# Performance work log

Hardware: AMD Instinct MI355X
Metric: run time of the kernel (lower is better)

Reference implementation:

```python
import jax, jax.numpy as jnp
import numpy as np

N_SEQ, T, IN, H, A = 256, 512, 128, 256, 32


def setup_inputs() -> dict:
    key = jax.random.key(0)
    ks = jax.random.split(key, 10)
    s = lambda k, sh: (jax.random.normal(k, sh, dtype=jnp.float32) * 0.05)
    features = jax.random.normal(ks[0], (N_SEQ * T, IN), dtype=jnp.float32)
    episode_starts = (jax.random.uniform(ks[1], (N_SEQ * T,)) < 0.02).astype(jnp.float32)
    h0 = jnp.zeros((1, N_SEQ, H), jnp.float32)
    c0 = jnp.zeros((1, N_SEQ, H), jnp.float32)
    return dict(
        features=features, episode_starts=episode_starts, h0=h0, c0=c0,
        W_ih=s(ks[2], (4 * H, IN)), W_hh=s(ks[3], (4 * H, H)),
        b_ih=s(ks[4], (4 * H,)), b_hh=s(ks[5], (4 * H,)),
        W_logit=s(ks[6], (A, H)), b_logit=s(ks[7], (A,)),
        W_value=s(ks[8], (1, H)), b_value=s(ks[9], (1,)),
    )


def _lstm_scan(x_seq, starts, h0, c0, W_ih, W_hh, b_ih, b_hh):
    # x_seq: (T, n_seq, IN); starts: (T, n_seq); h0/c0: (n_seq, H)
    # Precompute input projection once (big GEMM), recurrence only does h @ W_hh.
    x_proj = jnp.einsum('tbi,gi->tbg', x_seq, W_ih) + b_ih + b_hh  # (T, n_seq, 4H)

    def step(carry, inp):
        h, c = carry
        xp, st = inp
        m = (1.0 - st)[:, None]          # reset states at episode starts
        h = h * m
        c = c * m
        gates = xp + h @ W_hh.T          # (n_seq, 4H)
        i, f, g, o = jnp.split(gates, 4, axis=-1)  # PyTorch gate order i,f,g,o
        c = jax.nn.sigmoid(f) * c + jax.nn.sigmoid(i) * jnp.tanh(g)
        h = jax.nn.sigmoid(o) * jnp.tanh(c)
        return (h, c), h

    (h, c), ys = jax.lax.scan(step, (h0, c0), (x_proj, starts))
    return ys, h, c


def reference(features, episode_starts, h0, c0, W_ih, W_hh, b_ih, b_hh,
              W_logit, b_logit, W_value, b_value):
    n_seq = h0.shape[1]
    in_size = W_ih.shape[1]
    x_seq = features.reshape(n_seq, -1, in_size).swapaxes(0, 1)   # (T, n_seq, IN)
    starts = episode_starts.reshape(n_seq, -1).swapaxes(0, 1)     # (T, n_seq)
    ys, h, c = _lstm_scan(x_seq, starts, h0[0], c0[0], W_ih, W_hh, b_ih, b_hh)
    out = ys.swapaxes(0, 1).reshape(-1, ys.shape[-1])             # (n_seq*T, H)
    logits = out @ W_logit.T + b_logit                            # (n_seq*T, A)
    value = out @ W_value.T + b_value                             # (n_seq*T, 1)
    return logits, value, h[None], c[None]
```

## Files before the change

kernel.cpp:

```cpp
#include <hip/hip_runtime.h>
#include <hip/hip_bf16.h>


typedef float f32x4 __attribute__((ext_vector_type(4)));
typedef int   i32x4 __attribute__((ext_vector_type(4)));
typedef short s16x8 __attribute__((ext_vector_type(8)));
typedef short s16x4 __attribute__((ext_vector_type(4)));
typedef unsigned short u16x4 __attribute__((ext_vector_type(4)));

#define L2E   1.44269504088896340736f
#define L2E2  2.88539008177792681472f

__device__ __forceinline__ float fexp2(float x) {
#if __has_builtin(__builtin_amdgcn_exp2f)
  return __builtin_amdgcn_exp2f(x);
#else
  float r; asm("v_exp_f32 %0, %1" : "=v"(r) : "v"(x)); return r;
#endif
}
__device__ __forceinline__ float frcp(float x) { return __builtin_amdgcn_rcpf(x); }
__device__ __forceinline__ float bf2f(unsigned short u) {
  return __uint_as_float(((unsigned)u) << 16);
}
__device__ __forceinline__ unsigned short f2bf(float f) {
  unsigned int b = __float_as_uint(f);
  return (unsigned short)((b + 0x7FFFu + ((b >> 16) & 1u)) >> 16);
}

__global__ void k0_quant(const float* __restrict__ Whh,
                         const float* __restrict__ Wlog,
                         const float* __restrict__ Wval,
                         signed char* __restrict__ Wq, float* __restrict__ wsc,
                         signed char* __restrict__ Wlq, float* __restrict__ lsc) {
  int r = blockIdx.x, l = threadIdx.x;
  const float* src; signed char* dst; float* sd;
  if (r < 1024) { src = Whh + (size_t)r * 256; dst = Wq + (size_t)r * 256; sd = wsc + r; }
  else {
    int hr = r - 1024;
    src = (hr < 32) ? (Wlog + (size_t)hr * 256) : Wval;
    dst = Wlq + (size_t)hr * 256; sd = lsc + hr;
  }
  f32x4 v = *(const f32x4*)(src + l * 4);
  float m = fmaxf(fmaxf(fabsf(v.x), fabsf(v.y)), fmaxf(fabsf(v.z), fabsf(v.w)));
  #pragma unroll
  for (int off = 32; off; off >>= 1) m = fmaxf(m, __shfl_xor(m, off));
  float inv = (m > 0.f) ? (127.f / m) : 0.f;
  int q0 = (int)rintf(v.x * inv), q1 = (int)rintf(v.y * inv);
  int q2 = (int)rintf(v.z * inv), q3 = (int)rintf(v.w * inv);
  unsigned int pk = (q0 & 255) | ((q1 & 255) << 8) | ((q2 & 255) << 16) | ((q3 & 255) << 24);
  *(unsigned int*)(dst + l * 4) = pk;
  if (l == 0) *sd = m * (1.f / 127.f);
}

__device__ __forceinline__ void k1_body(int gk, char* smem,
                                        const float* __restrict__ feat,
                                        const float* __restrict__ Wih,
                                        const float* __restrict__ bih,
                                        const float* __restrict__ bhh,
                                        unsigned short* __restrict__ xp, int t0) {
  short (*Bl)[136] = (short (*)[136])smem;
  float* bias = (float*)(smem + 34816);
  const int tid = threadIdx.x;
  const int bm = gk >> 3, bn = gk & 7;
  const int m0 = bm << 7, j0 = bn << 5;
  const int tg = t0 + (bm >> 1), sbase = (bm & 1) << 7;
  #pragma unroll
  for (int it = 0; it < 8; ++it) {
    int idx = it * 512 + tid;
    int rr = idx >> 5, c4 = (idx & 31) << 2;
    int g = ((rr & 3) << 8) + j0 + (rr >> 2);
    f32x4 v = *(const f32x4*)(Wih + (size_t)g * 128 + c4);
    s16x4 pk = { (short)f2bf(v.x), (short)f2bf(v.y), (short)f2bf(v.z), (short)f2bf(v.w) };
    *(s16x4*)&Bl[rr][c4] = pk;
  }
  if (tid < 128) {
    int g = ((tid & 3) << 8) + j0 + (tid >> 2);
    bias[tid] = bih[g] + bhh[g];
  }
  const int w = tid >> 6, l = tid & 63;
  const int lr = l & 15, lk8 = (l >> 4) << 3;
  s16x8 a[4];
  {
    const float* fp = feat + ((size_t)(sbase + (w << 4) + lr) * 512 + tg) * 128 + lk8;
    #pragma unroll
    for (int kk = 0; kk < 4; ++kk) {
      f32x4 v0 = *(const f32x4*)(fp + kk * 32);
      f32x4 v1 = *(const f32x4*)(fp + kk * 32 + 4);
      s16x8 pk = { (short)f2bf(v0.x), (short)f2bf(v0.y), (short)f2bf(v0.z), (short)f2bf(v0.w),
                   (short)f2bf(v1.x), (short)f2bf(v1.y), (short)f2bf(v1.z), (short)f2bf(v1.w) };
      a[kk] = pk;
    }
  }
  __syncthreads();
  f32x4 z = {0.f, 0.f, 0.f, 0.f};
  f32x4 acc[8];
  #pragma unroll
  for (int nt = 0; nt < 8; ++nt) acc[nt] = z;
  #pragma unroll
  for (int kk = 0; kk < 4; ++kk) {
    #pragma unroll
    for (int nt = 0; nt < 8; ++nt) {
      s16x8 bb = *(const s16x8*)&Bl[nt * 16 + lr][kk * 32 + lk8];
      acc[nt] = __builtin_amdgcn_mfma_f32_16x16x32_bf16(a[kk], bb, acc[nt], 0, 0, 0);
    }
  }
  #pragma unroll
  for (int nt = 0; nt < 8; ++nt) {
    #pragma unroll
    for (int r = 0; r < 4; ++r) {
      int m = m0 + (w << 4) + (l >> 4) * 4 + r;
      int c = nt * 16 + lr;
      float gsc = ((c & 3) == 2) ? L2E2 : -L2E;
      float val = (acc[nt][r] + bias[c]) * gsc;
      xp[(size_t)m * 1024 + (j0 << 2) + c] = f2bf(val);
    }
  }
}

__device__ __forceinline__ void k2_body(int bid, char* smem,
                                        const unsigned short* __restrict__ xp,
                                        const signed char* __restrict__ Wq,
                                        const float* __restrict__ wsc,
                                        const float* __restrict__ ep,
                                        const float* __restrict__ h0,
                                        const float* __restrict__ c0,
                                        float* __restrict__ hstate,
                                        float* __restrict__ cstate,
                                        signed char* __restrict__ hbuf,
                                        float* __restrict__ out, int t0, int tc) {
  __builtin_amdgcn_s_setprio(3);
  signed char (*Hl)[4][272] = (signed char (*)[4][272])smem;
  float* flgl = (float*)(smem + 2176);
  const int tid = threadIdx.x;
  const int w = tid >> 6, l = tid & 63;
  const int lc = l & 15, lq = l >> 4;
  const int hf = lq >> 1;
  const int odd = lq & 1;
  const int sb2 = odd << 1;
  const int j = (w << 5) + (hf << 4) + lc;
  const int s0 = bid << 2;
  const bool last = (t0 + tc == 512);

  {
    const float* hsrc = (t0 == 0) ? h0 : hstate;
    #pragma unroll
    for (int it = 0; it < 2; ++it) {
      int idx = it * 512 + tid;
      int s = idx >> 8, jj = idx & 255;
      float v = hsrc[(size_t)(s0 + s) * 256 + jj];
      float q = rintf(fminf(fmaxf(v * 127.f, -127.f), 127.f));
      Hl[0][s][jj] = (signed char)(int)q;
    }
  }
  {
    int n = tc << 2;
    for (int idx = tid; idx < n; idx += 512) {
      int s = idx & 3, llt = idx >> 2;
      flgl[idx] = ep[(size_t)(s0 + s) * 512 + t0 + llt];
    }
  }

  i32x4 wq[8][4];
  #pragma unroll
  for (int tau = 0; tau < 8; ++tau) {
    int g = (tau >> 1) * 256 + (w << 5) + ((tau & 1) << 4) + lc;
    #pragma unroll
    for (int kk = 0; kk < 4; ++kk)
      wq[tau][kk] = *(const i32x4*)(Wq + (size_t)g * 256 + kk * 64 + (lq << 4));
  }
  float dsc[4];
  #pragma unroll
  for (int gamma = 0; gamma < 4; ++gamma) {
    float sgn = (gamma == 2) ? L2E2 : -L2E;
    dsc[gamma] = sgn * wsc[gamma * 256 + j] * (1.f / 127.f);
  }

  float cst[2];
  {
    const float* csrc = (t0 == 0) ? c0 : cstate;
    #pragma unroll
    for (int cc = 0; cc < 2; ++cc)
      cst[cc] = csrc[(size_t)(s0 + sb2 + cc) * 256 + j];
  }

  const size_t xoff = ((size_t)(s0 + sb2) * 256 + j) * 4;
  u16x4 xqA[2], xqB[2];
  {
    const unsigned short* pp = xp + xoff;
    #pragma unroll
    for (int cc = 0; cc < 2; ++cc) xqA[cc] = *(const u16x4*)(pp + cc * 1024);
  }
  __syncthreads();

  const int aoff = (lc & 3) * 272 + (lq << 4);
  const i32x4 zero4 = {0, 0, 0, 0};

#define STEP(HR, HWR, XC, XN, LT)                                              \
  {                                                                            \
    const int lt_ = (LT);                                                      \
    if (lt_ + 1 < tc) {                     \
      const unsigned short* pp = xp + (size_t)(lt_ + 1) * 262144 + xoff;       \
      _Pragma("unroll")                                                        \
      for (int cc = 0; cc < 2; ++cc) XN[cc] = *(const u16x4*)(pp + cc * 1024); \
    }                                                                          \
    float fa = flgl[lt_ * 4 + (lc & 3)];          \
    i32x4 racc[8];                                                             \
    const signed char* hbase = &(HR)[0][0];                                    \
    {                                                                          \
      i32x4 a = *(const i32x4*)(hbase + aoff);                                 \
      i32x4 am = (fa != 0.f) ? zero4 : a;                                      \
      _Pragma("unroll")                                                        \
      for (int tau = 0; tau < 8; ++tau)                                        \
        racc[tau] = __builtin_amdgcn_mfma_i32_16x16x64_i8(am, wq[tau][0], zero4, 0, 0, 0); \
    }                                                                          \
    _Pragma("unroll")                                                          \
    for (int kk = 1; kk < 4; ++kk) {                                           \
      i32x4 a = *(const i32x4*)(hbase + aoff + kk * 64);                       \
      i32x4 am = (fa != 0.f) ? zero4 : a;                                      \
      _Pragma("unroll")                                                        \
      for (int tau = 0; tau < 8; ++tau)                                        \
        racc[tau] = __builtin_amdgcn_mfma_i32_16x16x64_i8(am, wq[tau][kk], racc[tau], 0, 0, 0); \
    }                                                                          \
    i32x4 sg0 = hf ? racc[1] : racc[0];         \
    i32x4 sg1 = hf ? racc[3] : racc[2];                                        \
    i32x4 sg2 = hf ? racc[5] : racc[4];                                        \
    i32x4 sg3 = hf ? racc[7] : racc[6];                                        \
    signed char* hw = &(HWR)[0][0];                                            \
    signed char* hb = hbuf + ((size_t)lt_ * 256 + (s0 + sb2)) * 256 + j;       \
    _Pragma("unroll")                                                          \
    for (int cc = 0; cc < 2; ++cc) {                                           \
      int g0 = odd ? sg0[2 + cc] : sg0[cc];                                    \
      int g1 = odd ? sg1[2 + cc] : sg1[cc];                                    \
      int g2 = odd ? sg2[2 + cc] : sg2[cc];                                    \
      int g3 = odd ? sg3[2 + cc] : sg3[cc];                                    \
      u16x4 xv = XC[cc];                                                       \
      float xi = fmaf((float)g0, dsc[0], bf2f(xv.x));                          \
      float xf = fmaf((float)g1, dsc[1], bf2f(xv.y));                          \
      float xg = fmaf((float)g2, dsc[2], bf2f(xv.z));                          \
      float xo = fmaf((float)g3, dsc[3], bf2f(xv.w));                          \
      float si = frcp(1.f + fexp2(xi));                                        \
      float sf = frcp(1.f + fexp2(xf));                                        \
      float so = frcp(1.f + fexp2(xo));                                        \
      float tg = fmaf(-2.f, frcp(1.f + fexp2(xg)), 1.f);                       \
      float fr = flgl[lt_ * 4 + sb2 + cc];                                     \
      float cp = (fr != 0.f) ? 0.f : cst[cc];                                  \
      float cn = fmaf(sf, cp, si * tg);                                        \
      cst[cc] = cn;                                                            \
      float th = fmaf(-2.f, frcp(1.f + fexp2(L2E2 * cn)), 1.f);                \
      float hn = so * th;                                                      \
      signed char q8 = (signed char)(int)rintf(hn * 127.f);                    \
      hw[(sb2 + cc) * 272 + j] = q8;                                           \
      hb[cc * 256] = q8;                                                       \
      if (lt_ == tc - 1) {                                                     \
        int sg = s0 + sb2 + cc;                                                \
        hstate[(size_t)sg * 256 + j] = hn;                                     \
        cstate[(size_t)sg * 256 + j] = cn;                                     \
        if (last) {                                                            \
          out[4325376 + (size_t)sg * 256 + j] = hn;                            \
          out[4390912 + (size_t)sg * 256 + j] = cn;                            \
        }                                                                      \
      }                                                                        \
    }                                                                          \
    asm volatile("s_waitcnt lgkmcnt(0)\n\ts_barrier" ::: "memory");            \
  }

  for (int lt = 0; lt < tc; lt += 2) {
    STEP(Hl[0], Hl[1], xqA, xqB, lt);
    STEP(Hl[1], Hl[0], xqB, xqA, lt + 1);
  }
#undef STEP
}

__device__ __forceinline__ void k3_body(int gk,
                                        const signed char* __restrict__ hbuf,
                                        const signed char* __restrict__ Wlq,
                                        const float* __restrict__ lsc,
                                        const float* __restrict__ blog,
                                        const float* __restrict__ bval,
                                        float* __restrict__ out,
                                        int t0, int tc, int tcsh) {
  const int w = threadIdx.x >> 6, l = threadIdx.x & 63;
  const int lc = l & 15, lq = l >> 4;
  const int tk = gk * 8 + w;
  const int pg = tk >> tcsh, lt = tk & (tc - 1);
  const int t = t0 + lt;
  const i32x4 zero4 = {0, 0, 0, 0};

  i32x4 dacc[3] = {zero4, zero4, zero4};
  #pragma unroll
  for (int kk = 0; kk < 4; ++kk) {
    i32x4 a = *(const i32x4*)(hbuf + ((size_t)lt * 256 + (pg << 4) + lc) * 256
                              + kk * 64 + (lq << 4));
    #pragma unroll
    for (int n = 0; n < 3; ++n) {
      int row = n * 16 + lc;
      i32x4 bf = (row < 33) ? *(const i32x4*)(Wlq + (size_t)row * 256 + kk * 64 + (lq << 4))
                            : zero4;
      dacc[n] = __builtin_amdgcn_mfma_i32_16x16x64_i8(a, bf, dacc[n], 0, 0, 0);
    }
  }
  #pragma unroll
  for (int n = 0; n < 2; ++n) {
    float dsn = lsc[n * 16 + lc] * (1.f / 127.f);
    float lbn = blog[n * 16 + lc];
    #pragma unroll
    for (int r = 0; r < 4; ++r) {
      int sg = (pg << 4) + lq * 4 + r;
      out[((size_t)sg * 512 + t) * 32 + n * 16 + lc] = fmaf((float)dacc[n][r], dsn, lbn);
    }
  }
  if (lc == 0) {
    float ds2 = lsc[32] * (1.f / 127.f);
    float b2 = bval[0];
    #pragma unroll
    for (int r = 0; r < 4; ++r) {
      int sg = (pg << 4) + lq * 4 + r;
      out[4194304 + (size_t)sg * 512 + t] = fmaf((float)dacc[2][r], ds2, b2);
    }
  }
}

__launch_bounds__(512, 2)
__global__ void mega(int nk2, int t0_2, const unsigned short* xp2, signed char* hb2,
                     int nk1, int t0_1, unsigned short* xp1,
                     int nk3, int t0_3, const signed char* hb3,
                     const float* feat, const float* Wih,
                     const float* bih, const float* bhh,
                     const signed char* Wq, const float* wsc,
                     const signed char* Wlq, const float* lsc,
                     const float* ep, const float* h0, const float* c0,
                     const float* blog, const float* bval,
                     float* hstate, float* cstate, float* out,
                     int tc, int tcsh) {
  __shared__ __align__(16) char smem[81920];
  int bid = (int)blockIdx.x;
  if (bid < nk2) {
    k2_body(bid, smem, xp2, Wq, wsc, ep, h0, c0, hstate, cstate, hb2, out, t0_2, tc);
  } else if (bid < nk2 + nk1) {
    k1_body(bid - nk2, smem, feat, Wih, bih, bhh, xp1, t0_1);
  } else {
    k3_body(bid - nk2 - nk1, hb3, Wlq, lsc, blog, bval, out, t0_3, tc, tcsh);
  }
}

extern "C" void kernel_launch(void* const* d_in, const int* in_sizes, int n_in,
                              void* d_out, int out_size, void* d_ws, size_t ws_size,
                              hipStream_t stream) {
  const float* feat = (const float*)d_in[0];
  const float* ep   = (const float*)d_in[1];
  const float* h0   = (const float*)d_in[2];
  const float* c0   = (const float*)d_in[3];
  const float* Wih  = (const float*)d_in[4];
  const float* Whh  = (const float*)d_in[5];
  const float* bih  = (const float*)d_in[6];
  const float* bhh  = (const float*)d_in[7];
  const float* Wlog = (const float*)d_in[8];
  const float* blog = (const float*)d_in[9];
  const float* Wval = (const float*)d_in[10];
  const float* bval = (const float*)d_in[11];
  float* out = (float*)d_out;
  char* ws = (char*)d_ws;
  signed char* Wq     = (signed char*)(ws + 0);
  float*       wsc    = (float*)      (ws + 262144);
  signed char* Wlq    = (signed char*)(ws + 266240);
  float*       lsc    = (float*)      (ws + 274688);
  float*       hstate = (float*)      (ws + 275456);
  float*       cstate = (float*)      (ws + 537600);

  int Tc = 128;
  while (Tc > 16 && (size_t)1048576 + (size_t)Tc * 1179648 > ws_size) Tc >>= 1;
  int tcsh = 31 - __builtin_clz(Tc);
  int nc = 512 / Tc;
  size_t xpsz = (size_t)Tc * 524288, hbsz = (size_t)Tc * 65536;
  unsigned short* xpb[2] = { (unsigned short*)(ws + 1048576),
                             (unsigned short*)(ws + 1048576 + xpsz) };
  signed char*    hbb[2] = { (signed char*)(ws + 1048576 + 2 * xpsz),
                             (signed char*)(ws + 1048576 + 2 * xpsz + hbsz) };
  const int NK1 = Tc * 16;
  const int NK3 = Tc * 2;
  const int NK2 = 64;

  hipLaunchKernelGGL(k0_quant, dim3(1057), dim3(64), 0, stream,
                     Whh, Wlog, Wval, Wq, wsc, Wlq, lsc);
  hipLaunchKernelGGL(mega, dim3(NK1), dim3(512), 0, stream,
                     0, 0, xpb[0], hbb[0],
                     NK1, 0, xpb[0],
                     0, 0, hbb[0],
                     feat, Wih, bih, bhh, Wq, wsc, Wlq, lsc, ep, h0, c0,
                     blog, bval, hstate, cstate, out, Tc, tcsh);
  for (int j = 0; j < nc; ++j) {
    int nk1 = (j + 1 < nc) ? NK1 : 0;
    int nk3 = (j >= 1) ? NK3 : 0;
    hipLaunchKernelGGL(mega, dim3(NK2 + nk1 + nk3), dim3(512), 0, stream,
                       NK2, j * Tc, xpb[j & 1], hbb[j & 1],
                       nk1, (j + 1) * Tc, xpb[(j + 1) & 1],
                       nk3, (j - 1) * Tc, hbb[(j + 1) & 1],
                       feat, Wih, bih, bhh, Wq, wsc, Wlq, lsc, ep, h0, c0,
                       blog, bval, hstate, cstate, out, Tc, tcsh);
  }
  hipLaunchKernelGGL(mega, dim3(NK3), dim3(512), 0, stream,
                     0, 0, xpb[0], hbb[0],
                     0, 0, xpb[0],
                     NK3, (nc - 1) * Tc, hbb[(nc - 1) & 1],
                     feat, Wih, bih, bhh, Wq, wsc, Wlq, lsc, ep, h0, c0,
                     blog, bval, hstate, cstate, out, Tc, tcsh);
}
```

Baseline: 613.2 us.

## Use 1024-thread blocks so each recurrent thread handles one gate column

Doubles the mega kernel's block size to 1024 threads. The recurrent LSTM body now gives each of 16 waves 16 hidden columns, holding 4 gate weight fragments per thread instead of 8 and one sequence's cell state instead of two, with no cross-half selection. The GEMM and head bodies simply idle the extra 512 threads. The aim is to cut the serial per-step latency of the recurrence. In exchange, occupancy drops to one block per CU, the barriers span twice as many waves, and half the threads sit unused in the other phases.

```diff
diff --git a/kernel.cpp b/kernel.cpp
--- a/kernel.cpp
+++ b/kernel.cpp
@@ -64,23 +64,23 @@
   const int bm = gk >> 3, bn = gk & 7;
   const int m0 = bm << 7, j0 = bn << 5;
   const int tg = t0 + (bm >> 1), sbase = (bm & 1) << 7;
-  #pragma unroll
-  for (int it = 0; it < 8; ++it) {
-    int idx = it * 512 + tid;
-    int rr = idx >> 5, c4 = (idx & 31) << 2;
-    int g = ((rr & 3) << 8) + j0 + (rr >> 2);
-    f32x4 v = *(const f32x4*)(Wih + (size_t)g * 128 + c4);
-    s16x4 pk = { (short)f2bf(v.x), (short)f2bf(v.y), (short)f2bf(v.z), (short)f2bf(v.w) };
-    *(s16x4*)&Bl[rr][c4] = pk;
-  }
-  if (tid < 128) {
-    int g = ((tid & 3) << 8) + j0 + (tid >> 2);
-    bias[tid] = bih[g] + bhh[g];
-  }
-  const int w = tid >> 6, l = tid & 63;
-  const int lr = l & 15, lk8 = (l >> 4) << 3;
   s16x8 a[4];
-  {
+  if (tid < 512) {
+    #pragma unroll
+    for (int it = 0; it < 8; ++it) {
+      int idx = it * 512 + tid;
+      int rr = idx >> 5, c4 = (idx & 31) << 2;
+      int g = ((rr & 3) << 8) + j0 + (rr >> 2);
+      f32x4 v = *(const f32x4*)(Wih + (size_t)g * 128 + c4);
+      s16x4 pk = { (short)f2bf(v.x), (short)f2bf(v.y), (short)f2bf(v.z), (short)f2bf(v.w) };
+      *(s16x4*)&Bl[rr][c4] = pk;
+    }
+    if (tid < 128) {
+      int g = ((tid & 3) << 8) + j0 + (tid >> 2);
+      bias[tid] = bih[g] + bhh[g];
+    }
+    const int w = tid >> 6, l = tid & 63;
+    const int lr = l & 15, lk8 = (l >> 4) << 3;
     const float* fp = feat + ((size_t)(sbase + (w << 4) + lr) * 512 + tg) * 128 + lk8;
     #pragma unroll
     for (int kk = 0; kk < 4; ++kk) {
@@ -92,6 +92,9 @@
     }
   }
   __syncthreads();
+  if (tid >= 512) return;
+  const int w = tid >> 6, l = tid & 63;
+  const int lr = l & 15, lk8 = (l >> 4) << 3;
   f32x4 z = {0.f, 0.f, 0.f, 0.f};
   f32x4 acc[8];
   #pragma unroll
@@ -134,62 +137,47 @@
   const int tid = threadIdx.x;
   const int w = tid >> 6, l = tid & 63;
   const int lc = l & 15, lq = l >> 4;
-  const int hf = lq >> 1;
-  const int odd = lq & 1;
-  const int sb2 = odd << 1;
-  const int j = (w << 5) + (hf << 4) + lc;
+  const int j = (w << 4) + lc;
   const int s0 = bid << 2;
   const bool last = (t0 + tc == 512);
 
   {
     const float* hsrc = (t0 == 0) ? h0 : hstate;
-    #pragma unroll
-    for (int it = 0; it < 2; ++it) {
-      int idx = it * 512 + tid;
-      int s = idx >> 8, jj = idx & 255;
-      float v = hsrc[(size_t)(s0 + s) * 256 + jj];
-      float q = rintf(fminf(fmaxf(v * 127.f, -127.f), 127.f));
-      Hl[0][s][jj] = (signed char)(int)q;
-    }
+    int s = tid >> 8, jj = tid & 255;
+    float v = hsrc[(size_t)(s0 + s) * 256 + jj];
+    float q = rintf(fminf(fmaxf(v * 127.f, -127.f), 127.f));
+    Hl[0][s][jj] = (signed char)(int)q;
   }
   {
     int n = tc << 2;
-    for (int idx = tid; idx < n; idx += 512) {
+    for (int idx = tid; idx < n; idx += 1024) {
       int s = idx & 3, llt = idx >> 2;
       flgl[idx] = ep[(size_t)(s0 + s) * 512 + t0 + llt];
     }
   }
 
-  i32x4 wq[8][4];
-  #pragma unroll
-  for (int tau = 0; tau < 8; ++tau) {
-    int g = (tau >> 1) * 256 + (w << 5) + ((tau & 1) << 4) + lc;
+  i32x4 wq[4][4];
+  #pragma unroll
+  for (int g = 0; g < 4; ++g)
     #pragma unroll
     for (int kk = 0; kk < 4; ++kk)
-      wq[tau][kk] = *(const i32x4*)(Wq + (size_t)g * 256 + kk * 64 + (lq << 4));
-  }
+      wq[g][kk] = *(const i32x4*)(Wq + (size_t)(g * 256 + j) * 256 + kk * 64 + (lq << 4));
   float dsc[4];
   #pragma unroll
-  for (int gamma = 0; gamma < 4; ++gamma) {
-    float sgn = (gamma == 2) ? L2E2 : -L2E;
-    dsc[gamma] = sgn * wsc[gamma * 256 + j] * (1.f / 127.f);
-  }
-
-  float cst[2];
+  for (int g = 0; g < 4; ++g) {
+    float sgn = (g == 2) ? L2E2 : -L2E;
+    dsc[g] = sgn * wsc[g * 256 + j] * (1.f / 127.f);
+  }
+
+  float cst;
   {
     const float* csrc = (t0 == 0) ? c0 : cstate;
-    #pragma unroll
-    for (int cc = 0; cc < 2; ++cc)
-      cst[cc] = csrc[(size_t)(s0 + sb2 + cc) * 256 + j];
-  }
-
-  const size_t xoff = ((size_t)(s0 + sb2) * 256 + j) * 4;
-  u16x4 xqA[2], xqB[2];
-  {
-    const unsigned short* pp = xp + xoff;
-    #pragma unroll
-    for (int cc = 0; cc < 2; ++cc) xqA[cc] = *(const u16x4*)(pp + cc * 1024);
-  }
+    cst = csrc[(size_t)(s0 + lq) * 256 + j];
+  }
+
+  const size_t xoff = ((size_t)(s0 + lq) * 256 + j) * 4;
+  u16x4 xqA, xqB;
+  xqA = *(const u16x4*)(xp + xoff);
   __syncthreads();
 
   const int aoff = (lc & 3) * 272 + (lq << 4);
@@ -198,67 +186,64 @@
 #define STEP(HR, HWR, XC, XN, LT)                                              \
   {                                                                            \
     const int lt_ = (LT);                                                      \
-    if (lt_ + 1 < tc) {                     \
-      const unsigned short* pp = xp + (size_t)(lt_ + 1) * 262144 + xoff;       \
-      _Pragma("unroll")                                                        \
-      for (int cc = 0; cc < 2; ++cc) XN[cc] = *(const u16x4*)(pp + cc * 1024); \
-    }                                                                          \
+    if (lt_ + 1 < tc)                       \
+      XN = *(const u16x4*)(xp + (size_t)(lt_ + 1) * 262144 + xoff);            \
     float fa = flgl[lt_ * 4 + (lc & 3)];          \
-    i32x4 racc[8];                                                             \
+    i32x4 racc[4];                                                             \
     const signed char* hbase = &(HR)[0][0];                                    \
     {                                                                          \
       i32x4 a = *(const i32x4*)(hbase + aoff);                                 \
       i32x4 am = (fa != 0.f) ? zero4 : a;                                      \
       _Pragma("unroll")                                                        \
-      for (int tau = 0; tau < 8; ++tau)                                        \
-        racc[tau] = __builtin_amdgcn_mfma_i32_16x16x64_i8(am, wq[tau][0], zero4, 0, 0, 0); \
+      for (int g = 0; g < 4; ++g)                                              \
+        racc[g] = __builtin_amdgcn_mfma_i32_16x16x64_i8(am, wq[g][0], zero4, 0, 0, 0); \
     }                                                                          \
     _Pragma("unroll")                                                          \
     for (int kk = 1; kk < 4; ++kk) {                                           \
       i32x4 a = *(const i32x4*)(hbase + aoff + kk * 64);                       \
       i32x4 am = (fa != 0.f) ? zero4 : a;                                      \
       _Pragma("unroll")                                                        \
-      for (int tau = 0; tau < 8; ++tau)                                        \
-        racc[tau] = __builtin_amdgcn_mfma_i32_16x16x64_i8(am, wq[tau][kk], racc[tau], 0, 0, 0); \
+      for (int g = 0; g < 4; ++g)                                              \
+        racc[g] = __builtin_amdgcn_mfma_i32_16x16x64_i8(am, wq[g][kk], racc[g], 0, 0, 0); \
     }                                                                          \
-    i32x4 sg0 = hf ? racc[1] : racc[0];         \
-    i32x4 sg1 = hf ? racc[3] : racc[2];                                        \
-    i32x4 sg2 = hf ? racc[5] : racc[4];                                        \
-    i32x4 sg3 = hf ? racc[7] : racc[6];                                        \
-    signed char* hw = &(HWR)[0][0];                                            \
-    signed char* hb = hbuf + ((size_t)lt_ * 256 + (s0 + sb2)) * 256 + j;       \
-    _Pragma("unroll")                                                          \
-    for (int cc = 0; cc < 2; ++cc) {                                           \
-      int g0 = odd ? sg0[2 + cc] : sg0[cc];                                    \
-      int g1 = odd ? sg1[2 + cc] : sg1[cc];                                    \
-      int g2 = odd ? sg2[2 + cc] : sg2[cc];                                    \
-      int g3 = odd ? sg3[2 + cc] : sg3[cc];                                    \
-      u16x4 xv = XC[cc];                                                       \
-      float xi = fmaf((float)g0, dsc[0], bf2f(xv.x));                          \
-      float xf = fmaf((float)g1, dsc[1], bf2f(xv.y));                          \
-      float xg = fmaf((float)g2, dsc[2], bf2f(xv.z));                          \
-      float xo = fmaf((float)g3, dsc[3], bf2f(xv.w));                          \
-      float si = frcp(1.f + fexp2(xi));                                        \
-      float sf = frcp(1.f + fexp2(xf));                                        \
-      float so = frcp(1.f + fexp2(xo));                                        \
-      float tg = fmaf(-2.f, frcp(1.f + fexp2(xg)), 1.f);                       \
-      float fr = flgl[lt_ * 4 + sb2 + cc];                                     \
-      float cp = (fr != 0.f) ? 0.f : cst[cc];                                  \
-      float cn = fmaf(sf, cp, si * tg);                                        \
-      cst[cc] = cn;                                                            \
-      float th = fmaf(-2.f, frcp(1.f + fexp2(L2E2 * cn)), 1.f);                \
-      float hn = so * th;                                                      \
-      signed char q8 = (signed char)(int)rintf(hn * 127.f);                    \
-      hw[(sb2 + cc) * 272 + j] = q8;                                           \
-      hb[cc * 256] = q8;                                                       \
-      if (lt_ == tc - 1) {                                                     \
-        int sg = s0 + sb2 + cc;                                                \
-        hstate[(size_t)sg * 256 + j] = hn;                                     \
-        cstate[(size_t)sg * 256 + j] = cn;                                     \
-        if (last) {                                                            \
-          out[4325376 + (size_t)sg * 256 + j] = hn;                            \
-          out[4390912 + (size_t)sg * 256 + j] = cn;                            \
-        }                                                                      \
+      \
+    int r01_0 = (lq & 1) ? racc[0][1] : racc[0][0];                            \
+    int r23_0 = (lq & 1) ? racc[0][3] : racc[0][2];                            \
+    int g0 = (lq & 2) ? r23_0 : r01_0;                                         \
+    int r01_1 = (lq & 1) ? racc[1][1] : racc[1][0];                            \
+    int r23_1 = (lq & 1) ? racc[1][3] : racc[1][2];                            \
+    int g1 = (lq & 2) ? r23_1 : r01_1;                                         \
+    int r01_2 = (lq & 1) ? racc[2][1] : racc[2][0];                            \
+    int r23_2 = (lq & 1) ? racc[2][3] : racc[2][2];                            \
+    int g2 = (lq & 2) ? r23_2 : r01_2;                                         \
+    int r01_3 = (lq & 1) ? racc[3][1] : racc[3][0];                            \
+    int r23_3 = (lq & 1) ? racc[3][3] : racc[3][2];                            \
+    int g3 = (lq & 2) ? r23_3 : r01_3;                                         \
+    u16x4 xv = XC;                                                             \
+    float xi = fmaf((float)g0, dsc[0], bf2f(xv.x));                            \
+    float xf = fmaf((float)g1, dsc[1], bf2f(xv.y));                            \
+    float xg = fmaf((float)g2, dsc[2], bf2f(xv.z));                            \
+    float xo = fmaf((float)g3, dsc[3], bf2f(xv.w));                            \
+    float si = frcp(1.f + fexp2(xi));                                          \
+    float sf = frcp(1.f + fexp2(xf));                                          \
+    float so = frcp(1.f + fexp2(xo));                                          \
+    float tg = fmaf(-2.f, frcp(1.f + fexp2(xg)), 1.f);                         \
+    float fr = flgl[lt_ * 4 + lq];                                             \
+    float cp = (fr != 0.f) ? 0.f : cst;                                        \
+    float cn = fmaf(sf, cp, si * tg);                                          \
+    cst = cn;                                                                  \
+    float th = fmaf(-2.f, frcp(1.f + fexp2(L2E2 * cn)), 1.f);                  \
+    float hn = so * th;                                                        \
+    signed char q8 = (signed char)(int)rintf(hn * 127.f);                      \
+    (&(HWR)[0][0])[lq * 272 + j] = q8;                                         \
+    hbuf[((size_t)lt_ * 256 + s0 + lq) * 256 + j] = q8;                        \
+    if (lt_ == tc - 1) {                                                       \
+      int sq = s0 + lq;                                                        \
+      hstate[(size_t)sq * 256 + j] = hn;                                       \
+      cstate[(size_t)sq * 256 + j] = cn;                                       \
+      if (last) {                                                              \
+        out[4325376 + (size_t)sq * 256 + j] = hn;                              \
+        out[4390912 + (size_t)sq * 256 + j] = cn;                              \
       }                                                                        \
     }                                                                          \
     asm volatile("s_waitcnt lgkmcnt(0)\n\ts_barrier" ::: "memory");            \
@@ -279,6 +264,7 @@
                                         const float* __restrict__ bval,
                                         float* __restrict__ out,
                                         int t0, int tc, int tcsh) {
+  if (threadIdx.x >= 512) return;
   const int w = threadIdx.x >> 6, l = threadIdx.x & 63;
   const int lc = l & 15, lq = l >> 4;
   const int tk = gk * 8 + w;
@@ -320,7 +306,7 @@
   }
 }
 
-__launch_bounds__(512, 2)
+__launch_bounds__(1024, 1)
 __global__ void mega(int nk2, int t0_2, const unsigned short* xp2, signed char* hb2,
                      int nk1, int t0_1, unsigned short* xp1,
                      int nk3, int t0_3, const signed char* hb3,
@@ -332,7 +318,7 @@
                      const float* blog, const float* bval,
                      float* hstate, float* cstate, float* out,
                      int tc, int tcsh) {
-  __shared__ __align__(16) char smem[81920];
+  __shared__ __align__(16) char smem[35840];
   int bid = (int)blockIdx.x;
   if (bid < nk2) {
     k2_body(bid, smem, xp2, Wq, wsc, ep, h0, c0, hstate, cstate, hb2, out, t0_2, tc);
@@ -382,7 +368,7 @@
 
   hipLaunchKernelGGL(k0_quant, dim3(1057), dim3(64), 0, stream,
                      Whh, Wlog, Wval, Wq, wsc, Wlq, lsc);
-  hipLaunchKernelGGL(mega, dim3(NK1), dim3(512), 0, stream,
+  hipLaunchKernelGGL(mega, dim3(NK1), dim3(1024), 0, stream,
                      0, 0, xpb[0], hbb[0],
                      NK1, 0, xpb[0],
                      0, 0, hbb[0],
@@ -391,14 +377,14 @@
   for (int j = 0; j < nc; ++j) {
     int nk1 = (j + 1 < nc) ? NK1 : 0;
     int nk3 = (j >= 1) ? NK3 : 0;
-    hipLaunchKernelGGL(mega, dim3(NK2 + nk1 + nk3), dim3(512), 0, stream,
+    hipLaunchKernelGGL(mega, dim3(NK2 + nk1 + nk3), dim3(1024), 0, stream,
                        NK2, j * Tc, xpb[j & 1], hbb[j & 1],
                        nk1, (j + 1) * Tc, xpb[(j + 1) & 1],
                        nk3, (j - 1) * Tc, hbb[(j + 1) & 1],
                        feat, Wih, bih, bhh, Wq, wsc, Wlq, lsc, ep, h0, c0,
                        blog, bval, hstate, cstate, out, Tc, tcsh);
   }
-  hipLaunchKernelGGL(mega, dim3(NK3), dim3(512), 0, stream,
+  hipLaunchKernelGGL(mega, dim3(NK3), dim3(1024), 0, stream,
                      0, 0, xpb[0], hbb[0],
                      0, 0, xpb[0],
                      NK3, (nc - 1) * Tc, hbb[(nc - 1) & 1],
```

After: 551.0 us. 10.1% less time.
